# Optimization experiments

Hardware: AMD Instinct MI355X
Metric: run time of the kernel (lower is better)

Reference implementation:

```python
import jax, jax.numpy as jnp
import numpy as np

T, IN, OUT, R = 8192, 4096, 4096, 64


def setup_inputs() -> dict:
    key = jax.random.key(0)
    ks = jax.random.split(key, 7)
    # signed int4 values in [-8, 8) for activations and (unpacked) weights
    quant_x = jax.random.randint(ks[0], (T, IN), -8, 8, dtype=jnp.int32)
    weight_q = jax.random.randint(ks[1], (OUT, IN), -8, 8, dtype=jnp.int32)
    # positive per-token / per-channel symmetric-quant scales
    scale_x = jax.random.uniform(ks[2], (T,), dtype=jnp.float32) * 0.01 + 1e-4
    weight_scales = jax.random.uniform(ks[3], (OUT,), dtype=jnp.float32) * 0.01 + 1e-4
    outlier_x = jax.random.normal(ks[4], (T, R), dtype=jnp.float32)
    w_outlier = jax.random.normal(ks[5], (OUT, R), dtype=jnp.float32)
    bias = jax.random.normal(ks[6], (OUT,), dtype=jnp.float32)
    return {"quant_x": quant_x, "weight_q": weight_q, "scale_x": scale_x,
            "weight_scales": weight_scales, "outlier_x": outlier_x,
            "w_outlier": w_outlier, "bias": bias}


def reference(quant_x, weight_q, scale_x, weight_scales, outlier_x, w_outlier, bias):
    acc = jnp.matmul(quant_x, weight_q.T)
    # sym_dequant: per-row activation scale * per-column weight scale
    x_out = acc.astype(jnp.float32) * scale_x[:, None] * weight_scales[None, :]
    # outlier low-rank addmm + bias epilogue
    x_out = x_out + jnp.matmul(outlier_x, w_outlier.T) + bias
    return x_out
```

## Files before the change

### kernel.cpp

```cpp
#include <hip/hip_runtime.h>

#define T_DIM 8192
#define IN_DIM 4096
#define OUT_DIM 4096
#define R_DIM 64
#define NKP 32

typedef int i32x4 __attribute__((ext_vector_type(4)));
typedef float f32x4 __attribute__((ext_vector_type(4)));
typedef _Float16 f16x8 __attribute__((ext_vector_type(8)));

__device__ __forceinline__ int pack4(int4 v) {
  return (v.x & 255) | ((v.y & 255) << 8) | ((v.z & 255) << 16) | ((unsigned)v.w << 24);
}

__device__ __forceinline__ void gload16(const void* g, void* l) {
  __builtin_amdgcn_global_load_lds(
      (const __attribute__((address_space(1))) void*)(unsigned long long)g,
      (__attribute__((address_space(3))) void*)(unsigned)(unsigned long long)l,
      16, 0, 0);
}

__device__ __forceinline__ i32x4 unp(int x, int y) {
  i32x4 r;
  r[0] = x & 0x0F0F0F0F;
  r[1] = (x >> 4) & 0x0F0F0F0F;
  r[2] = y & 0x0F0F0F0F;
  r[3] = (y >> 4) & 0x0F0F0F0F;
  return r;
}

__device__ __forceinline__ unsigned pb(int a, int b) {
  return (unsigned)(a + 8) | ((unsigned)(b + 8) << 4);
}

__global__ __launch_bounds__(256)
void cvt_pack_kernel(const int* __restrict__ qx, const int* __restrict__ wq,
                     char* __restrict__ pk, int* __restrict__ SS) {
  const int wave = blockIdx.x * 4 + (threadIdx.x >> 6);
  const int l = threadIdx.x & 63;
  const int nw = gridDim.x * 4;
  for (int r = wave; r < T_DIM + OUT_DIM; r += nw) {
    const int* src = (r < T_DIM) ? (qx + (size_t)r * IN_DIM)
                                 : (wq + (size_t)(r - T_DIM) * IN_DIM);
    const int4* src4 = (const int4*)src;
    char* dst = pk + (size_t)r * 2048;
    const int rx = (r >> 1) & 3;
    int s = 0;
#pragma unroll
    for (int i = 0; i < 4; ++i) {
      const int q = i * 64 + l;
      const int kt = q >> 2, g = q & 3;
      int4 s0 = src4[q * 4 + 0], s1 = src4[q * 4 + 1];
      int4 s2 = src4[q * 4 + 2], s3 = src4[q * 4 + 3];
      s += s0.x + s0.y + s0.z + s0.w + s1.x + s1.y + s1.z + s1.w +
           s2.x + s2.y + s2.z + s2.w + s3.x + s3.y + s3.z + s3.w;
      unsigned dw0 = pb(s0.x, s0.y) | (pb(s0.z, s0.w) << 8) |
                     (pb(s1.x, s1.y) << 16) | (pb(s1.z, s1.w) << 24);
      unsigned dw1 = pb(s2.x, s2.y) | (pb(s2.z, s2.w) << 8) |
                     (pb(s3.x, s3.y) << 16) | (pb(s3.z, s3.w) << 24);
      const int off = (kt >> 1) * 64 + ((g ^ rx) << 4) + (kt & 1) * 8;
      *(uint2*)(dst + off) = make_uint2(dw0, dw1);
    }
#pragma unroll
    for (int off = 1; off < 64; off <<= 1) s += __shfl_xor(s, off, 64);
    if (l == 0) SS[r] = s + 8 * IN_DIM;
  }
}

__global__ __launch_bounds__(256, 4)
void w4a4_gemm(const char* __restrict__ A8, const char* __restrict__ B8,
               const int* __restrict__ SS,
               const float* __restrict__ sx, const float* __restrict__ sw,
               const float* __restrict__ ox, const float* __restrict__ ow,
               const float* __restrict__ bias, float* __restrict__ out) {
  __shared__ __align__(16) char smem[32768];

  const int bid = blockIdx.x;
  const int xcd = bid & 7, c = bid >> 3;
  const int tn = (xcd & 3) * 8 + (c & 7);
  const int tm = (xcd >> 2) * 32 + (c >> 3);
  const int brow = tm * 128, bcol = tn * 128;

  const int t = threadIdx.x;
  const int w = t >> 6, l = t & 63;
  const int wr = w >> 1, wc = w & 1;
  const int l16 = l & 15, lk = l >> 4;

  const char* gA0 = A8 + (size_t)(brow + (t >> 2)) * 2048 + (t & 3) * 16;
  const char* gA1 = gA0 + (size_t)64 * 2048;
  const char* gB0 = B8 + (size_t)(bcol + (t >> 2)) * 2048 + (t & 3) * 16;
  const char* gB1 = gB0 + (size_t)64 * 2048;
  char* const dA0 = smem + t * 16;
  char* const dA1 = smem + 4096 + t * 16;
  char* const dB0 = smem + 8192 + t * 16;
  char* const dB1 = smem + 12288 + t * 16;

  const int Ra = wr * 64 + l16;
  const int Cb = wc * 64 + l16;
  const char* aR = smem + Ra * 64 + ((lk ^ ((Ra >> 1) & 3)) << 4);
  const char* bR = smem + 8192 + Cb * 64 + ((lk ^ ((Cb >> 1) & 3)) << 4);

  i32x4 acc[4][4];
#pragma unroll
  for (int m = 0; m < 4; ++m)
#pragma unroll
    for (int n = 0; n < 4; ++n) acc[m][n] = (i32x4){0, 0, 0, 0};

  auto stage = [&](int kp) {
    const int off = kp << 6;
    const int buf = (kp & 1) << 14;
    gload16(gA0 + off, dA0 + buf);
    gload16(gA1 + off, dA1 + buf);
    gload16(gB0 + off, dB0 + buf);
    gload16(gB1 + off, dB1 + buf);
  };

  auto compute = [&](int kp) {
    const int buf = (kp & 1) << 14;
    const char* sa = aR + buf;
    const char* sb = bR + buf;
    i32x4 ap[4], bp[4];
#pragma unroll
    for (int m = 0; m < 4; ++m) ap[m] = *(const i32x4*)(sa + m * 1024);
#pragma unroll
    for (int n = 0; n < 4; ++n) bp[n] = *(const i32x4*)(sb + n * 1024);
    i32x4 bv[4];
#pragma unroll
    for (int n = 0; n < 4; ++n) bv[n] = unp(bp[n][0], bp[n][1]);
    __builtin_amdgcn_s_setprio(1);
#pragma unroll
    for (int m = 0; m < 4; ++m) {
      i32x4 av = unp(ap[m][0], ap[m][1]);
      acc[m][0] = __builtin_amdgcn_mfma_i32_16x16x64_i8(av, bv[0], acc[m][0], 0, 0, 0);
      acc[m][1] = __builtin_amdgcn_mfma_i32_16x16x64_i8(av, bv[1], acc[m][1], 0, 0, 0);
      acc[m][2] = __builtin_amdgcn_mfma_i32_16x16x64_i8(av, bv[2], acc[m][2], 0, 0, 0);
      acc[m][3] = __builtin_amdgcn_mfma_i32_16x16x64_i8(av, bv[3], acc[m][3], 0, 0, 0);
    }
    __builtin_amdgcn_s_setprio(0);
#pragma unroll
    for (int n = 0; n < 4; ++n) bv[n] = unp(bp[n][2], bp[n][3]);
    __builtin_amdgcn_s_setprio(1);
#pragma unroll
    for (int m = 0; m < 4; ++m) {
      i32x4 av = unp(ap[m][2], ap[m][3]);
      acc[m][0] = __builtin_amdgcn_mfma_i32_16x16x64_i8(av, bv[0], acc[m][0], 0, 0, 0);
      acc[m][1] = __builtin_amdgcn_mfma_i32_16x16x64_i8(av, bv[1], acc[m][1], 0, 0, 0);
      acc[m][2] = __builtin_amdgcn_mfma_i32_16x16x64_i8(av, bv[2], acc[m][2], 0, 0, 0);
      acc[m][3] = __builtin_amdgcn_mfma_i32_16x16x64_i8(av, bv[3], acc[m][3], 0, 0, 0);
    }
    __builtin_amdgcn_s_setprio(0);
  };

  stage(0);
  for (int kp = 0; kp < NKP; ++kp) {
    asm volatile("s_waitcnt vmcnt(0)" ::: "memory");
    __builtin_amdgcn_s_barrier();
    __builtin_amdgcn_sched_barrier(0);
    if (kp < NKP - 1) stage(kp + 1);
    compute(kp);
  }

  const int orow0 = brow + wr * 64 + (lk << 2);
  const int ocol0 = bcol + wc * 64 + l16;
  const int* SA = SS;
  const int* SB = SS + T_DIM;
  float swv[4], bvv[4];
  int cb[4];
#pragma unroll
  for (int n = 0; n < 4; ++n) {
    swv[n] = sw[ocol0 + n * 16];
    bvv[n] = bias[ocol0 + n * 16];
    cb[n] = -8 * SB[ocol0 + n * 16];
  }

  f32x4 facc[4][4];
#pragma unroll
  for (int m = 0; m < 4; ++m) {
#pragma unroll
    for (int r = 0; r < 4; ++r) {
      const int row = orow0 + m * 16 + r;
      const float sxv = sx[row];
      const int ca = 262144 - 8 * SA[row];
#pragma unroll
      for (int n = 0; n < 4; ++n)
        facc[m][n][r] = (float)(acc[m][n][r] + ca + cb[n]) * sxv * swv[n];
    }
  }

  __syncthreads();
#pragma unroll
  for (int j = 0; j < 4; ++j) {
    int q = j * 256 + t;
    int row = q >> 3, cd = q & 7, cs = cd ^ (row & 7);
    const float* ga = ox + (size_t)(brow + row) * R_DIM + cs * 8;
    float4 f0 = *(const float4*)ga, f1 = *(const float4*)(ga + 4);
    f16x8 h;
    h[0] = (_Float16)f0.x; h[1] = (_Float16)f0.y; h[2] = (_Float16)f0.z; h[3] = (_Float16)f0.w;
    h[4] = (_Float16)f1.x; h[5] = (_Float16)f1.y; h[6] = (_Float16)f1.z; h[7] = (_Float16)f1.w;
    *(f16x8*)(smem + row * 128 + cd * 16) = h;
    const float* gb = ow + (size_t)(bcol + row) * R_DIM + cs * 8;
    f0 = *(const float4*)gb; f1 = *(const float4*)(gb + 4);
    f16x8 g;
    g[0] = (_Float16)f0.x; g[1] = (_Float16)f0.y; g[2] = (_Float16)f0.z; g[3] = (_Float16)f0.w;
    g[4] = (_Float16)f1.x; g[5] = (_Float16)f1.y; g[6] = (_Float16)f1.z; g[7] = (_Float16)f1.w;
    *(f16x8*)(smem + 16384 + row * 128 + cd * 16) = g;
  }
  __syncthreads();

  const char* qa = smem + (wr * 64 + l16) * 128;
  const char* qb = smem + 16384 + (wc * 64 + l16) * 128;
  const int x7 = l16 & 7;
#pragma unroll
  for (int s = 0; s < 2; ++s) {
    const int ca2 = ((s * 4 + lk) ^ x7) << 4;
    f16x8 hb[4];
#pragma unroll
    for (int n = 0; n < 4; ++n) hb[n] = *(const f16x8*)(qb + n * 2048 + ca2);
#pragma unroll
    for (int m = 0; m < 4; ++m) {
      f16x8 ha = *(const f16x8*)(qa + m * 2048 + ca2);
#pragma unroll
      for (int n = 0; n < 4; ++n)
        facc[m][n] = __builtin_amdgcn_mfma_f32_16x16x32_f16(ha, hb[n], facc[m][n], 0, 0, 0);
    }
  }

#pragma unroll
  for (int m = 0; m < 4; ++m)
#pragma unroll
    for (int r = 0; r < 4; ++r) {
      float* po = out + (size_t)(orow0 + m * 16 + r) * OUT_DIM + ocol0;
#pragma unroll
      for (int n = 0; n < 4; ++n) po[n * 16] = facc[m][n][r] + bvv[n];
    }
}

__global__ __launch_bounds__(256)
void w4a4_gemm_fb(const int* __restrict__ A32, const int* __restrict__ B32,
                  const float* __restrict__ sx, const float* __restrict__ sw,
                  const float* __restrict__ ox, const float* __restrict__ ow,
                  const float* __restrict__ bias, float* __restrict__ out) {
  __shared__ __align__(16) unsigned char smem[32768];
  char* sA = (char*)smem;
  char* sB = (char*)smem + 8192;

  const int bid = blockIdx.x;
  const int swzb = (bid & 7) * 256 + (bid >> 3);
  const int tm = swzb >> 5, tn = swzb & 31;
  const int brow = tm * 128, bcol = tn * 128;

  const int t = threadIdx.x;
  const int l = t & 63;
  const int wr = (t >> 6) >> 1, wc = (t >> 6) & 1;
  const int l16 = l & 15, lk = l >> 4;

  i32x4 iacc[4][4];
#pragma unroll
  for (int m = 0; m < 4; ++m)
#pragma unroll
    for (int n = 0; n < 4; ++n) iacc[m][n] = (i32x4){0, 0, 0, 0};

  const int ar = t >> 2;
  const int ac = (t & 3) << 4;
  const int* hA0 = A32 + (size_t)(brow + ar) * IN_DIM + ac;
  const int* hA1 = hA0 + (size_t)64 * IN_DIM;
  const int* hB0 = B32 + (size_t)(bcol + ar) * IN_DIM + ac;
  const int* hB1 = hB0 + (size_t)64 * IN_DIM;

  const char* fragA = sA + (size_t)(wr * 64 + l16) * 64 + lk * 16;
  const char* fragB = sB + (size_t)(wc * 64 + l16) * 64 + lk * 16;

  for (int k0 = 0; k0 < IN_DIM; k0 += 64) {
    const int4* pA0 = (const int4*)(hA0 + k0);
    int4 r0 = {pack4(pA0[0]), pack4(pA0[1]), pack4(pA0[2]), pack4(pA0[3])};
    *(int4*)(sA + t * 16) = r0;
    const int4* pA1 = (const int4*)(hA1 + k0);
    int4 r1 = {pack4(pA1[0]), pack4(pA1[1]), pack4(pA1[2]), pack4(pA1[3])};
    *(int4*)(sA + 4096 + t * 16) = r1;
    const int4* pB0 = (const int4*)(hB0 + k0);
    int4 r2 = {pack4(pB0[0]), pack4(pB0[1]), pack4(pB0[2]), pack4(pB0[3])};
    *(int4*)(sB + t * 16) = r2;
    const int4* pB1 = (const int4*)(hB1 + k0);
    int4 r3 = {pack4(pB1[0]), pack4(pB1[1]), pack4(pB1[2]), pack4(pB1[3])};
    *(int4*)(sB + 4096 + t * 16) = r3;
    __syncthreads();
    i32x4 av[4], bv[4];
#pragma unroll
    for (int m = 0; m < 4; ++m) av[m] = *(const i32x4*)(fragA + m * 1024);
#pragma unroll
    for (int n = 0; n < 4; ++n) bv[n] = *(const i32x4*)(fragB + n * 1024);
#pragma unroll
    for (int m = 0; m < 4; ++m)
#pragma unroll
      for (int n = 0; n < 4; ++n)
        iacc[m][n] = __builtin_amdgcn_mfma_i32_16x16x64_i8(av[m], bv[n], iacc[m][n], 0, 0, 0);
    __syncthreads();
  }

  const int orow = brow + wr * 64 + lk * 4;
  const int ocol = bcol + wc * 64 + l16;
  float swv[4], bvv[4];
#pragma unroll
  for (int n = 0; n < 4; ++n) { swv[n] = sw[ocol + n * 16]; bvv[n] = bias[ocol + n * 16]; }

  f32x4 facc[4][4];
#pragma unroll
  for (int m = 0; m < 4; ++m)
#pragma unroll
    for (int r = 0; r < 4; ++r) {
      float sxv = sx[orow + m * 16 + r];
#pragma unroll
      for (int n = 0; n < 4; ++n) facc[m][n][r] = (float)iacc[m][n][r] * sxv * swv[n];
    }

  _Float16* oA = (_Float16*)smem;
  _Float16* oB = (_Float16*)(smem + 16384);
#pragma unroll
  for (int j = 0; j < 4; ++j) {
    int c = j * 256 + t;
    int rr2 = c >> 3, c8 = (c & 7) << 3;
    const float* gp = ox + (size_t)(brow + rr2) * R_DIM + c8;
    float4 f0 = *(const float4*)gp;
    float4 f1 = *(const float4*)(gp + 4);
    f16x8 h;
    h[0] = (_Float16)f0.x; h[1] = (_Float16)f0.y; h[2] = (_Float16)f0.z; h[3] = (_Float16)f0.w;
    h[4] = (_Float16)f1.x; h[5] = (_Float16)f1.y; h[6] = (_Float16)f1.z; h[7] = (_Float16)f1.w;
    *(f16x8*)((char*)oA + (size_t)c * 16) = h;
    const float* gq = ow + (size_t)(bcol + rr2) * R_DIM + c8;
    f0 = *(const float4*)gq; f1 = *(const float4*)(gq + 4);
    f16x8 g;
    g[0] = (_Float16)f0.x; g[1] = (_Float16)f0.y; g[2] = (_Float16)f0.z; g[3] = (_Float16)f0.w;
    g[4] = (_Float16)f1.x; g[5] = (_Float16)f1.y; g[6] = (_Float16)f1.z; g[7] = (_Float16)f1.w;
    *(f16x8*)((char*)oB + (size_t)c * 16) = g;
  }
  __syncthreads();

  const char* qa = (const char*)oA + (size_t)(wr * 64 + l16) * 128 + lk * 16;
  const char* qb = (const char*)oB + (size_t)(wc * 64 + l16) * 128 + lk * 16;
#pragma unroll
  for (int s = 0; s < 2; ++s) {
    f16x8 ha[4], hb[4];
#pragma unroll
    for (int m = 0; m < 4; ++m) ha[m] = *(const f16x8*)(qa + m * 2048 + s * 64);
#pragma unroll
    for (int n = 0; n < 4; ++n) hb[n] = *(const f16x8*)(qb + n * 2048 + s * 64);
#pragma unroll
    for (int m = 0; m < 4; ++m)
#pragma unroll
      for (int n = 0; n < 4; ++n)
        facc[m][n] = __builtin_amdgcn_mfma_f32_16x16x32_f16(ha[m], hb[n], facc[m][n], 0, 0, 0);
  }

#pragma unroll
  for (int m = 0; m < 4; ++m)
#pragma unroll
    for (int r = 0; r < 4; ++r) {
      float* po = out + (size_t)(orow + m * 16 + r) * OUT_DIM + ocol;
#pragma unroll
      for (int n = 0; n < 4; ++n) po[n * 16] = facc[m][n][r] + bvv[n];
    }
}

extern "C" void kernel_launch(void* const* d_in, const int* in_sizes, int n_in,
                              void* d_out, int out_size, void* d_ws, size_t ws_size,
                              hipStream_t stream) {
  const int*   qx   = (const int*)d_in[0];
  const int*   wq   = (const int*)d_in[1];
  const float* sx   = (const float*)d_in[2];
  const float* sw   = (const float*)d_in[3];
  const float* ox   = (const float*)d_in[4];
  const float* ow   = (const float*)d_in[5];
  const float* bias = (const float*)d_in[6];
  float* out = (float*)d_out;

  const size_t packedA = (size_t)T_DIM * 2048;
  const size_t packedB = (size_t)OUT_DIM * 2048;
  const size_t ssBytes = (size_t)(T_DIM + OUT_DIM) * 4;
  const size_t need = packedA + packedB + ssBytes;

  if (ws_size >= need) {
    char* pk = (char*)d_ws;
    int* SS = (int*)(pk + packedA + packedB);
    cvt_pack_kernel<<<768, 256, 0, stream>>>(qx, wq, pk, SS);
    w4a4_gemm<<<2048, 256, 0, stream>>>(pk, pk + packedA, SS, sx, sw, ox, ow, bias, out);
  } else {
    w4a4_gemm_fb<<<2048, 256, 0, stream>>>(qx, wq, sx, sw, ox, ow, bias, out);
  }
}
```

Measured before the change: 175.4 us.

## Give each wave private LDS tiles and drop block barriers from GEMM loop

Each of the four waves now loads its own 64-row A and 64-column B slices into a private 16KB LDS region, so the per-iteration block barrier is gone and waves only wait on their own vmcnt. The loop prefetches two k-steps ahead, using vmcnt(8) to let one stage stay in flight. The cost is duplicated global loads, since A and B slices are each fetched by two waves, plus doubled LDS (64KB), which lowers occupancy to 2 blocks per CU.

```diff
diff --git a/kernel.cpp b/kernel.cpp
--- a/kernel.cpp
+++ b/kernel.cpp
@@ -68,13 +68,13 @@
   }
 }
 
-__global__ __launch_bounds__(256, 4)
+__global__ __launch_bounds__(256, 2)
 void w4a4_gemm(const char* __restrict__ A8, const char* __restrict__ B8,
                const int* __restrict__ SS,
                const float* __restrict__ sx, const float* __restrict__ sw,
                const float* __restrict__ ox, const float* __restrict__ ow,
                const float* __restrict__ bias, float* __restrict__ out) {
-  __shared__ __align__(16) char smem[32768];
+  __shared__ __align__(16) char smem[65536];
 
   const int bid = blockIdx.x;
   const int xcd = bid & 7, c = bid >> 3;
@@ -87,19 +87,14 @@
   const int wr = w >> 1, wc = w & 1;
   const int l16 = l & 15, lk = l >> 4;
 
-  const char* gA0 = A8 + (size_t)(brow + (t >> 2)) * 2048 + (t & 3) * 16;
-  const char* gA1 = gA0 + (size_t)64 * 2048;
-  const char* gB0 = B8 + (size_t)(bcol + (t >> 2)) * 2048 + (t & 3) * 16;
-  const char* gB1 = gB0 + (size_t)64 * 2048;
-  char* const dA0 = smem + t * 16;
-  char* const dA1 = smem + 4096 + t * 16;
-  char* const dB0 = smem + 8192 + t * 16;
-  char* const dB1 = smem + 12288 + t * 16;
-
-  const int Ra = wr * 64 + l16;
-  const int Cb = wc * 64 + l16;
-  const char* aR = smem + Ra * 64 + ((lk ^ ((Ra >> 1) & 3)) << 4);
-  const char* bR = smem + 8192 + Cb * 64 + ((lk ^ ((Cb >> 1) & 3)) << 4);
+  const char* gA = A8 + (size_t)(brow + wr * 64 + (l >> 2)) * 2048 + (l & 3) * 16;
+  const char* gB = B8 + (size_t)(bcol + wc * 64 + (l >> 2)) * 2048 + (l & 3) * 16;
+  char* const wbase = smem + w * 16384;
+  char* const dst0 = wbase + l * 16;
+
+  const int xo = (lk ^ ((l16 >> 1) & 3)) << 4;
+  const char* aR = wbase + l16 * 64 + xo;
+  const char* bR = wbase + 4096 + l16 * 64 + xo;
 
   i32x4 acc[4][4];
 #pragma unroll
@@ -109,15 +104,16 @@
 
   auto stage = [&](int kp) {
     const int off = kp << 6;
-    const int buf = (kp & 1) << 14;
-    gload16(gA0 + off, dA0 + buf);
-    gload16(gA1 + off, dA1 + buf);
-    gload16(gB0 + off, dB0 + buf);
-    gload16(gB1 + off, dB1 + buf);
+    char* d = dst0 + ((kp & 1) << 13);
+#pragma unroll
+    for (int j = 0; j < 4; ++j) {
+      gload16(gA + (size_t)j * 16 * 2048 + off, d + j * 1024);
+      gload16(gB + (size_t)j * 16 * 2048 + off, d + 4096 + j * 1024);
+    }
   };
 
   auto compute = [&](int kp) {
-    const int buf = (kp & 1) << 14;
+    const int buf = (kp & 1) << 13;
     const char* sa = aR + buf;
     const char* sb = bR + buf;
     i32x4 ap[4], bp[4];
@@ -152,14 +148,18 @@
     __builtin_amdgcn_s_setprio(0);
   };
 
-  stage(0);
-  for (int kp = 0; kp < NKP; ++kp) {
-    asm volatile("s_waitcnt vmcnt(0)" ::: "memory");
-    __builtin_amdgcn_s_barrier();
+  stage(0); stage(1);
+  for (int kp = 0; kp < NKP - 1; ++kp) {
+    asm volatile("s_waitcnt vmcnt(8)" ::: "memory");
     __builtin_amdgcn_sched_barrier(0);
-    if (kp < NKP - 1) stage(kp + 1);
     compute(kp);
-  }
+    asm volatile("s_waitcnt lgkmcnt(0)" ::: "memory");
+    __builtin_amdgcn_sched_barrier(0);
+    if (kp + 2 < NKP) stage(kp + 2);
+  }
+  asm volatile("s_waitcnt vmcnt(0)" ::: "memory");
+  __builtin_amdgcn_sched_barrier(0);
+  compute(NKP - 1);
 
   const int orow0 = brow + wr * 64 + (lk << 2);
   const int ocol0 = bcol + wc * 64 + l16;
```

New measurement: 192.2 us. +9.6%, slower.
